# Optimization experiments

Measured on AMD Instinct MI355X. Metric: run time of the kernel, lower is better.

Reference implementation:

```python
import jax, jax.numpy as jnp
import numpy as np

N, H, B = 8192, 32, 4          # points, hypotheses, scenes
C0, C1, CF = 128, 128, 64      # scale-0 chans, scale-1 chans, pts_feat chans
HID = 256                      # h_dim
D0, D1 = 24, 48                # voxel grid sides per scale
EPS = 1e-5


def setup_inputs() -> dict:
    key = jax.random.key(0)
    ks = jax.random.split(key, 30)
    nrm = lambda k, s, sc=1.0: jax.random.normal(k, s, jnp.float32) * sc
    in_dim = C0 + C1 + CF
    inp = {
        'pts': jax.random.uniform(ks[0], (N, H, 3), jnp.float32),
        'pts_feat': nrm(ks[1], (N, H, CF)),
        'pts_batch': jax.random.randint(ks[2], (N,), 0, B),
        'vol0': nrm(ks[3], (B, C0, D0, D0, D0)),
        'vol1': nrm(ks[4], (B, C1, D1, D1, D1)),
        'w0': nrm(ks[5], (HID, in_dim, 3), 1.0 / np.sqrt(in_dim * 3)),
        'w1': nrm(ks[6], (HID, HID, 3), 1.0 / np.sqrt(HID * 3)),
        'w2': nrm(ks[7], (HID, HID, 3), 1.0 / np.sqrt(HID * 3)),
        'w3': nrm(ks[8], (1, HID, 3), 1.0 / np.sqrt(HID * 3)),
        'b3': jnp.zeros((1,), jnp.float32),
    }
    for i in range(3):
        k = jax.random.split(ks[9 + i], 4)
        inp[f'g{i}'] = 1.0 + 0.1 * nrm(k[0], (HID,))
        inp[f'b{i}'] = 0.1 * nrm(k[1], (HID,))
        inp[f'm{i}'] = 0.1 * nrm(k[2], (HID,))
        inp[f'v{i}'] = jax.random.uniform(k[3], (HID,), jnp.float32, 0.5, 1.5)
    return inp


def _trilinear(vol, coords, batch):
    """vol [B,C,X,Y,Z], coords [Q,3] in voxel units, batch [Q] -> [Q,C].
    Zero padding outside the grid; align_corners=True semantics."""
    Bv, C, X, Y, Z = vol.shape
    v = jnp.transpose(vol, (0, 2, 3, 4, 1))  # [B,X,Y,Z,C] channels-last gather
    dims = jnp.array([X, Y, Z], jnp.int32)
    f = jnp.floor(coords)
    frac = coords - f
    fi = f.astype(jnp.int32)
    out = jnp.zeros((coords.shape[0], C), vol.dtype)
    for dx in (0, 1):
        for dy in (0, 1):
            for dz in (0, 1):
                off = jnp.array([dx, dy, dz], jnp.int32)
                idx = fi + off
                valid = jnp.all((idx >= 0) & (idx < dims), axis=1)
                ic = jnp.clip(idx, 0, dims - 1)
                w = ((frac[:, 0] if dx else 1.0 - frac[:, 0]) *
                     (frac[:, 1] if dy else 1.0 - frac[:, 1]) *
                     (frac[:, 2] if dz else 1.0 - frac[:, 2]))
                g = v[batch, ic[:, 0], ic[:, 1], ic[:, 2]]  # [Q,C] irregular gather
                out = out + (w * valid.astype(w.dtype))[:, None] * g
    return out


def _conv1d(x, w):
    return jax.lax.conv_general_dilated(x, w, (1,), [(1, 1)],
                                        dimension_numbers=('NCH', 'OIH', 'NCH'))


def _bn(x, g, b, m, v):
    return (x - m[:, None]) * (g[:, None] / jnp.sqrt(v[:, None] + EPS)) + b[:, None]


def reference(pts, pts_feat, pts_batch, vol0, vol1,
              w0, g0, b0, m0, v0, w1, g1, b1, m1, v1,
              w2, g2, b2, m2, v2, w3, b3):
    n_pts, n_hyp = pts.shape[0], pts.shape[1]
    q = pts.reshape(-1, 3)                      # [N*H, 3], normalized [0,1]
    bidx = jnp.repeat(pts_batch, n_hyp)         # [N*H]
    f0 = _trilinear(vol0, q * (D0 - 1), bidx).reshape(n_pts, n_hyp, -1)
    f1 = _trilinear(vol1, q * (D1 - 1), bidx).reshape(n_pts, n_hyp, -1)
    # loop concatenation order: cat(f1, cat(f0, pts_feat))
    features = jnp.concatenate([f1, f0, pts_feat], axis=2)  # [N,H,320]
    x = jnp.transpose(features, (0, 2, 1))      # [N, 320, H]
    x = jax.nn.relu(_bn(_conv1d(x, w0), g0, b0, m0, v0))
    x = jax.nn.relu(_bn(_conv1d(x, w1), g1, b1, m1, v1))
    x = jax.nn.relu(_bn(_conv1d(x, w2), g2, b2, m2, v2))
    x = _conv1d(x, w3) + b3[None, :, None]      # [N,1,H]
    return jax.nn.softmax(x[:, 0, :], axis=1)   # [N,H]
```

## Files before the change

kernel.cpp:

```cpp
#include <hip/hip_runtime.h>


typedef _Float16 half8 __attribute__((ext_vector_type(8)));
typedef float floatx16 __attribute__((ext_vector_type(16)));

#define NPTS  8192
#define HH    32
#define GPTS  4
#define PITCH 324
#define S1    110592
#define S0    13824
#define EPSF  1e-5f

__global__ void tvol_h(const float* __restrict__ in, ushort* __restrict__ out, int S) {
    __shared__ float t[32][33];
    const int b  = blockIdx.z;
    const int s0 = blockIdx.x * 32, c0 = blockIdx.y * 32;
    const int tx = threadIdx.x & 31, ty = threadIdx.x >> 5;
    const float* ip = in + ((size_t)b * 128 + c0) * S + s0;
#pragma unroll
    for (int j = 0; j < 32; j += 8)
        t[ty + j][tx] = ip[(size_t)(ty + j) * S + tx];
    __syncthreads();
    ushort* op = out + ((size_t)b * S + s0) * 128 + c0;
#pragma unroll
    for (int j = 0; j < 32; j += 8)
        op[(size_t)(ty + j) * 128 + tx] = __builtin_bit_cast(ushort, (_Float16)t[tx][ty + j]);
}

__global__ void wprep(const float* __restrict__ w, ushort* __restrict__ dst, int I, int KC) {
    int tid = blockIdx.x * 256 + threadIdx.x;
    if (tid >= KC * 4096) return;
    int j    = tid & 7;
    int lane = (tid >> 3) & 63;
    int nt   = (tid >> 9) & 7;
    int kc   = tid >> 12;
    int I16  = I / 16;
    int o    = nt * 32 + (lane & 31);
    int t    = kc / I16;
    int iw   = (kc % I16) * 16 + (lane >> 5) * 8 + j;
    float v  = w[((size_t)o * I + iw) * 3 + t];
    dst[tid] = __builtin_bit_cast(ushort, (_Float16)v);
}

__device__ __forceinline__ void setup_corners(float px, float py, float pz, int D,
                                              int* __restrict__ idx, float* __restrict__ wt) {
    float cx = px * (D - 1), cy = py * (D - 1), cz = pz * (D - 1);
    float fx = floorf(cx), fy = floorf(cy), fz = floorf(cz);
    float rx = cx - fx, ry = cy - fy, rz = cz - fz;
    int ix = (int)fx, iy = (int)fy, iz = (int)fz;
#pragma unroll
    for (int k = 0; k < 8; ++k) {
        int dx = k >> 2, dy = (k >> 1) & 1, dz = k & 1;
        int jx = ix + dx, jy = iy + dy, jz = iz + dz;
        bool valid = (jx >= 0) && (jx < D) && (jy >= 0) && (jy < D) && (jz >= 0) && (jz < D);
        int cxi = min(max(jx, 0), D - 1), cyi = min(max(jy, 0), D - 1), czi = min(max(jz, 0), D - 1);
        float w = (dx ? rx : 1.f - rx) * (dy ? ry : 1.f - ry) * (dz ? rz : 1.f - rz);
        idx[k] = (cxi * D + cyi) * D + czi;
        wt[k]  = valid ? w : 0.f;
    }
}

__device__ __forceinline__ uint packh2(float a, float b) {
    ushort ua = __builtin_bit_cast(ushort, (_Float16)a);
    ushort ub = __builtin_bit_cast(ushort, (_Float16)b);
    return (uint)ua | ((uint)ub << 16);
}

__device__ __forceinline__ half8 lda(const ushort* p) {
    uint2 lo = *(const uint2*)p;
    uint2 hi = *(const uint2*)(p + 4);
    uint4 u; u.x = lo.x; u.y = lo.y; u.z = hi.x; u.w = hi.y;
    return __builtin_bit_cast(half8, u);
}

template <int I16>
__device__ __forceinline__ void conv_layer(
    ushort (&F)[GPTS][34][PITCH], const ushort* __restrict__ wf,
    const float* __restrict__ gg, const float* __restrict__ bb,
    const float* __restrict__ mm, const float* __restrict__ vv,
    int wv, int lane)
{
    constexpr int KC = 3 * I16;
    const int ch = wv * 32 + (lane & 31);
    const float sc = gg[ch] / sqrtf(vv[ch] + EPSF);
    const float bs = bb[ch] - mm[ch] * sc;

    floatx16 acc[GPTS];
#pragma unroll
    for (int p = 0; p < GPTS; ++p)
#pragma unroll
        for (int r = 0; r < 16; ++r) acc[p][r] = 0.f;

    const ushort* aB = &F[0][0][0] + (lane & 31) * PITCH + (lane >> 5) * 8;
    const ushort* bB = wf + (size_t)wv * 512 + (size_t)lane * 8;

    half8 p0 = *(const half8*)(bB);
    half8 p1 = *(const half8*)(bB + 1 * 4096);
    half8 p2 = *(const half8*)(bB + 2 * 4096);
    half8 p3 = *(const half8*)(bB + 3 * 4096);

    int t = 0, ic = 0;
#define STEP(BREG, KNEXT)                                                        \
    {                                                                            \
        const ushort* ap = aB + t * PITCH + ic * 16;                             \
        half8 a0 = lda(ap);                                                      \
        half8 a1 = lda(ap + 1 * 34 * PITCH);                                     \
        half8 a2 = lda(ap + 2 * 34 * PITCH);                                     \
        half8 a3 = lda(ap + 3 * 34 * PITCH);                                     \
        acc[0] = __builtin_amdgcn_mfma_f32_32x32x16_f16(a0, BREG, acc[0], 0, 0, 0); \
        acc[1] = __builtin_amdgcn_mfma_f32_32x32x16_f16(a1, BREG, acc[1], 0, 0, 0); \
        acc[2] = __builtin_amdgcn_mfma_f32_32x32x16_f16(a2, BREG, acc[2], 0, 0, 0); \
        acc[3] = __builtin_amdgcn_mfma_f32_32x32x16_f16(a3, BREG, acc[3], 0, 0, 0); \
        BREG = *(const half8*)(bB + (size_t)min(KNEXT, KC - 1) * 4096);          \
        if (++ic == I16) { ic = 0; ++t; }                                        \
    }

#pragma unroll 1
    for (int kc = 0; kc < KC; kc += 4) {
        STEP(p0, kc + 4)
        STEP(p1, kc + 5)
        STEP(p2, kc + 6)
        STEP(p3, kc + 7)
    }
#undef STEP

    __syncthreads();
#pragma unroll
    for (int p = 0; p < GPTS; ++p)
#pragma unroll
        for (int r = 0; r < 16; ++r) {
            int h = (r & 3) + 8 * (r >> 2) + 4 * (lane >> 5);
            float v = fmaxf(fmaf(acc[p][r], sc, bs), 0.f);
            F[p][h + 1][ch] = __builtin_bit_cast(ushort, (_Float16)v);
        }
    __syncthreads();
}

__global__ __launch_bounds__(512, 2) void fused_kernel(
    const float* __restrict__ pts, const float* __restrict__ pf,
    const int* __restrict__ pbatch,
    const ushort* __restrict__ v1t, const ushort* __restrict__ v0t,
    const ushort* __restrict__ wf0, const ushort* __restrict__ wf1,
    const ushort* __restrict__ wf2,
    const float* __restrict__ w3, const float* __restrict__ b3,
    const float* __restrict__ g0, const float* __restrict__ be0,
    const float* __restrict__ m0, const float* __restrict__ va0,
    const float* __restrict__ g1, const float* __restrict__ be1,
    const float* __restrict__ m1, const float* __restrict__ va1,
    const float* __restrict__ g2, const float* __restrict__ be2,
    const float* __restrict__ m2, const float* __restrict__ va2,
    float* __restrict__ outp)
{
    __shared__ ushort F[GPTS][34][PITCH];
    __shared__ float  w3s[768];

    const int tid = threadIdx.x, lane = tid & 63, wv = tid >> 6;

    if (tid < 256) {
        w3s[tid]       = w3[tid];
        w3s[256 + tid] = w3[256 + tid];
        w3s[512 + tid] = w3[512 + tid];
    }

    for (int i = tid; i < 162 * GPTS; i += 512) {
        int p = i / 162, c = i - p * 162;
        ((uint*)&F[p][0][0])[c]  = 0u;
        ((uint*)&F[p][33][0])[c] = 0u;
    }

    {
        const int g = tid >> 2, cj = tid & 3;
        const int pt = g >> 5, h = g & 31;
        const int n = blockIdx.x * GPTS + pt;
        const float* pp = pts + ((size_t)n * HH + h) * 3;
        const float px = pp[0], py = pp[1], pz = pp[2];
        const int bi = pbatch[n];
        int idx1[8]; float wt1[8]; setup_corners(px, py, pz, 48, idx1, wt1);
        int idx0[8]; float wt0[8]; setup_corners(px, py, pz, 24, idx0, wt0);

        {
            const ushort* vb = v1t + (size_t)bi * (128ull * S1) + cj * 32;
            float acc[32];
#pragma unroll
            for (int k = 0; k < 32; ++k) acc[k] = 0.f;
#pragma unroll
            for (int c = 0; c < 8; ++c) {
                const half8* p = (const half8*)(vb + (size_t)idx1[c] * 128);
                float w = wt1[c];
#pragma unroll
                for (int q = 0; q < 4; ++q) {
                    half8 x = p[q];
#pragma unroll
                    for (int e = 0; e < 8; ++e) acc[q * 8 + e] += w * (float)x[e];
                }
            }
            ushort* fr = &F[pt][h + 1][cj * 32];
#pragma unroll
            for (int k = 0; k < 8; ++k) {
                uint2 u; u.x = packh2(acc[4 * k], acc[4 * k + 1]);
                u.y = packh2(acc[4 * k + 2], acc[4 * k + 3]);
                ((uint2*)fr)[k] = u;
            }
        }
        {
            const ushort* vb = v0t + (size_t)bi * (128ull * S0) + cj * 32;
            float acc[32];
#pragma unroll
            for (int k = 0; k < 32; ++k) acc[k] = 0.f;
#pragma unroll
            for (int c = 0; c < 8; ++c) {
                const half8* p = (const half8*)(vb + (size_t)idx0[c] * 128);
                float w = wt0[c];
#pragma unroll
                for (int q = 0; q < 4; ++q) {
                    half8 x = p[q];
#pragma unroll
                    for (int e = 0; e < 8; ++e) acc[q * 8 + e] += w * (float)x[e];
                }
            }
            ushort* fr = &F[pt][h + 1][128 + cj * 32];
#pragma unroll
            for (int k = 0; k < 8; ++k) {
                uint2 u; u.x = packh2(acc[4 * k], acc[4 * k + 1]);
                u.y = packh2(acc[4 * k + 2], acc[4 * k + 3]);
                ((uint2*)fr)[k] = u;
            }
        }
        {
            const float* pfp = pf + ((size_t)n * HH + h) * 64 + cj * 16;
            ushort* fr = &F[pt][h + 1][256 + cj * 16];
#pragma unroll
            for (int k = 0; k < 4; ++k) {
                float4 v = *(const float4*)(pfp + 4 * k);
                uint2 u; u.x = packh2(v.x, v.y); u.y = packh2(v.z, v.w);
                ((uint2*)fr)[k] = u;
            }
        }
    }
    __syncthreads();

    conv_layer<20>(F, wf0, g0, be0, m0, va0, wv, lane);
    conv_layer<16>(F, wf1, g1, be1, m1, va1, wv, lane);
    conv_layer<16>(F, wf2, g2, be2, m2, va2, wv, lane);

    if (wv < GPTS) {
        const int hh = lane & 31, ihalf = lane >> 5;
        float a = 0.f;
#pragma unroll
        for (int t = 0; t < 3; ++t) {
            const ushort* fr = &F[wv][hh + t][ihalf * 128];
#pragma unroll
            for (int b8 = 0; b8 < 16; ++b8) {
                half8 x = lda(fr + b8 * 8);
                int i0 = ihalf * 128 + b8 * 8;
#pragma unroll
                for (int j = 0; j < 8; ++j)
                    a += (float)x[j] * w3s[(i0 + j) * 3 + t];
            }
        }
        a += __shfl_xor(a, 32, 64);
        a += b3[0];
        float mx = a;
#pragma unroll
        for (int m = 16; m >= 1; m >>= 1) mx = fmaxf(mx, __shfl_xor(mx, m, 64));
        float e = expf(a - mx);
        float s = e;
#pragma unroll
        for (int m = 16; m >= 1; m >>= 1) s += __shfl_xor(s, m, 64);
        if (lane < 32)
            outp[((size_t)(blockIdx.x * GPTS + wv)) * HH + hh] = e / s;
    }
}

extern "C" void kernel_launch(void* const* d_in, const int* in_sizes, int n_in,
                              void* d_out, int out_size, void* d_ws, size_t ws_size,
                              hipStream_t stream) {
    const float* pts      = (const float*)d_in[0];
    const float* pts_feat = (const float*)d_in[1];
    const int*   pbatch   = (const int*)d_in[2];
    const float* vol0     = (const float*)d_in[3];
    const float* vol1     = (const float*)d_in[4];
    const float* w0 = (const float*)d_in[5];
    const float* w1 = (const float*)d_in[6];
    const float* w2 = (const float*)d_in[7];
    const float* w3 = (const float*)d_in[8];
    const float* b3 = (const float*)d_in[9];
    const float* g0 = (const float*)d_in[10];
    const float* be0 = (const float*)d_in[11];
    const float* m0 = (const float*)d_in[12];
    const float* va0 = (const float*)d_in[13];
    const float* g1 = (const float*)d_in[14];
    const float* be1 = (const float*)d_in[15];
    const float* m1 = (const float*)d_in[16];
    const float* va1 = (const float*)d_in[17];
    const float* g2 = (const float*)d_in[18];
    const float* be2 = (const float*)d_in[19];
    const float* m2 = (const float*)d_in[20];
    const float* va2 = (const float*)d_in[21];
    float* outp = (float*)d_out;

    const size_t o_v1 = 0;
    const size_t s_v1 = 4ull * S1 * 128;
    const size_t o_v0 = o_v1 + s_v1;
    const size_t s_v0 = 4ull * S0 * 128;
    const size_t o_w0 = o_v0 + s_v0;
    const size_t s_w0 = 60ull * 4096;
    const size_t o_w1 = o_w0 + s_w0;
    const size_t s_w1 = 48ull * 4096;
    const size_t o_w2 = o_w1 + s_w1;
    const size_t s_w2 = 48ull * 4096;
    const size_t need = (o_w2 + s_w2) * 2 + 65536;
    if (ws_size < need) return;

    ushort* wsu = (ushort*)d_ws;
    ushort* v1t = wsu + o_v1;
    ushort* v0t = wsu + o_v0;
    ushort* wf0 = wsu + o_w0;
    ushort* wf1 = wsu + o_w1;
    ushort* wf2 = wsu + o_w2;

    tvol_h<<<dim3(S1 / 32, 4, 4), 256, 0, stream>>>(vol1, v1t, S1);
    tvol_h<<<dim3(S0 / 32, 4, 4), 256, 0, stream>>>(vol0, v0t, S0);
    wprep<<<(int)((60 * 4096 + 255) / 256), 256, 0, stream>>>(w0, wf0, 320, 60);
    wprep<<<(int)((48 * 4096 + 255) / 256), 256, 0, stream>>>(w1, wf1, 256, 48);
    wprep<<<(int)((48 * 4096 + 255) / 256), 256, 0, stream>>>(w2, wf2, 256, 48);

    fused_kernel<<<NPTS / GPTS, 512, 0, stream>>>(
        pts, pts_feat, pbatch, v1t, v0t, wf0, wf1, wf2, w3, b3,
        g0, be0, m0, va0, g1, be1, m1, va1, g2, be2, m2, va2, outp);
}
```

Measured before the change: 1.002 ms.

## Split gather from conv into separate kernels, shrink LDS tile for occupancy

Trilinear gathers and the pts_feat conversion move out of the fused kernel into a dedicated gather kernel that writes fp16 features to a workspace buffer, processed in chunks sized to the workspace. The conv kernel now handles 3 points per block with a padded pitch, 16-byte LDS loads and launch bounds allowing 4 blocks per CU, trading a global round-trip of the feature tensor for higher occupancy and no gather stalls inside the MFMA kernel. The volume transpose kernel is also rewritten to convert to fp16 before the LDS stage and emit 16-byte stores.

```diff
diff --git a/kernel.cpp b/kernel.cpp
--- a/kernel.cpp
+++ b/kernel.cpp
@@ -6,26 +6,42 @@
 
 #define NPTS  8192
 #define HH    32
-#define GPTS  4
-#define PITCH 324
+#define GPTS  3
+#define PITCH 328
+#define ROWS  34
 #define S1    110592
 #define S0    13824
 #define EPSF  1e-5f
 
-__global__ void tvol_h(const float* __restrict__ in, ushort* __restrict__ out, int S) {
-    __shared__ float t[32][33];
-    const int b  = blockIdx.z;
-    const int s0 = blockIdx.x * 32, c0 = blockIdx.y * 32;
-    const int tx = threadIdx.x & 31, ty = threadIdx.x >> 5;
-    const float* ip = in + ((size_t)b * 128 + c0) * S + s0;
-#pragma unroll
-    for (int j = 0; j < 32; j += 8)
-        t[ty + j][tx] = ip[(size_t)(ty + j) * S + tx];
+__global__ __launch_bounds__(256) void tvol2(const float* __restrict__ in,
+                                             ushort* __restrict__ out, int S) {
+    __shared__ uint t[64][65];
+    const int b  = blockIdx.y;
+    const int s0 = blockIdx.x * 64;
+    const int tid = threadIdx.x;
+    const int l = tid & 63, cp0 = tid >> 6;
+#pragma unroll
+    for (int rep = 0; rep < 16; ++rep) {
+        int cpi = cp0 + 4 * rep;
+        int c0 = 2 * cpi;
+        float x0 = in[((size_t)b * 128 + c0) * S + s0 + l];
+        float x1 = in[((size_t)b * 128 + c0 + 1) * S + s0 + l];
+        ushort u0 = __builtin_bit_cast(ushort, (_Float16)x0);
+        ushort u1 = __builtin_bit_cast(ushort, (_Float16)x1);
+        t[l][cpi] = (uint)u0 | ((uint)u1 << 16);
+    }
     __syncthreads();
-    ushort* op = out + ((size_t)b * S + s0) * 128 + c0;
-#pragma unroll
-    for (int j = 0; j < 32; j += 8)
-        op[(size_t)(ty + j) * 128 + tx] = __builtin_bit_cast(ushort, (_Float16)t[tx][ty + j]);
+    const int s = tid >> 2, qd = tid & 3;
+    uint4* op = (uint4*)(out + ((size_t)b * S + s0 + s) * 128 + qd * 32);
+#pragma unroll
+    for (int j = 0; j < 4; ++j) {
+        uint4 v;
+        v.x = t[s][qd * 16 + 4 * j + 0];
+        v.y = t[s][qd * 16 + 4 * j + 1];
+        v.z = t[s][qd * 16 + 4 * j + 2];
+        v.w = t[s][qd * 16 + 4 * j + 3];
+        op[j] = v;
+    }
 }
 
 __global__ void wprep(const float* __restrict__ w, ushort* __restrict__ dst, int I, int KC) {
@@ -67,16 +83,103 @@
     return (uint)ua | ((uint)ub << 16);
 }
 
-__device__ __forceinline__ half8 lda(const ushort* p) {
-    uint2 lo = *(const uint2*)p;
-    uint2 hi = *(const uint2*)(p + 4);
-    uint4 u; u.x = lo.x; u.y = lo.y; u.z = hi.x; u.w = hi.y;
+__device__ __forceinline__ half8 lda16(const ushort* p) {
+    uint4 u = *(const uint4*)p;
     return __builtin_bit_cast(half8, u);
+}
+
+__global__ __launch_bounds__(256, 4) void gather_kernel(
+    const float* __restrict__ pts, const float* __restrict__ pf,
+    const int* __restrict__ pbatch,
+    const ushort* __restrict__ v1t, const ushort* __restrict__ v0t,
+    ushort* __restrict__ Fg, int q0)
+{
+    const int gid  = blockIdx.x * 256 + threadIdx.x;
+    const int qrel = gid >> 2, cj = gid & 3;
+    const int q    = q0 + qrel;
+    const int n    = q >> 5;
+
+    const float* pp = pts + (size_t)q * 3;
+    const float px = pp[0], py = pp[1], pz = pp[2];
+    const int bi = pbatch[n];
+
+    int idx1[8]; float wt1[8]; setup_corners(px, py, pz, 48, idx1, wt1);
+    int idx0[8]; float wt0[8]; setup_corners(px, py, pz, 24, idx0, wt0);
+
+    ushort* dq = Fg + (size_t)qrel * 320;
+
+    {
+        const ushort* vb = v1t + (size_t)bi * (128ull * S1) + cj * 32;
+        float acc[32];
+#pragma unroll
+        for (int k = 0; k < 32; ++k) acc[k] = 0.f;
+#pragma unroll
+        for (int c = 0; c < 8; ++c) {
+            const ushort* p = vb + (size_t)idx1[c] * 128;
+            float w = wt1[c];
+#pragma unroll
+            for (int qd = 0; qd < 4; ++qd) {
+                half8 x = lda16(p + 8 * qd);
+#pragma unroll
+                for (int e = 0; e < 8; ++e) acc[qd * 8 + e] += w * (float)x[e];
+            }
+        }
+        uint4* d = (uint4*)(dq + cj * 32);
+#pragma unroll
+        for (int j = 0; j < 4; ++j) {
+            uint4 u;
+            u.x = packh2(acc[8 * j + 0], acc[8 * j + 1]);
+            u.y = packh2(acc[8 * j + 2], acc[8 * j + 3]);
+            u.z = packh2(acc[8 * j + 4], acc[8 * j + 5]);
+            u.w = packh2(acc[8 * j + 6], acc[8 * j + 7]);
+            d[j] = u;
+        }
+    }
+    {
+        const ushort* vb = v0t + (size_t)bi * (128ull * S0) + cj * 32;
+        float acc[32];
+#pragma unroll
+        for (int k = 0; k < 32; ++k) acc[k] = 0.f;
+#pragma unroll
+        for (int c = 0; c < 8; ++c) {
+            const ushort* p = vb + (size_t)idx0[c] * 128;
+            float w = wt0[c];
+#pragma unroll
+            for (int qd = 0; qd < 4; ++qd) {
+                half8 x = lda16(p + 8 * qd);
+#pragma unroll
+                for (int e = 0; e < 8; ++e) acc[qd * 8 + e] += w * (float)x[e];
+            }
+        }
+        uint4* d = (uint4*)(dq + 128 + cj * 32);
+#pragma unroll
+        for (int j = 0; j < 4; ++j) {
+            uint4 u;
+            u.x = packh2(acc[8 * j + 0], acc[8 * j + 1]);
+            u.y = packh2(acc[8 * j + 2], acc[8 * j + 3]);
+            u.z = packh2(acc[8 * j + 4], acc[8 * j + 5]);
+            u.w = packh2(acc[8 * j + 6], acc[8 * j + 7]);
+            d[j] = u;
+        }
+    }
+    {
+        const float* pfp = pf + (size_t)q * 64 + cj * 16;
+        uint4* d = (uint4*)(dq + 256 + cj * 16);
+#pragma unroll
+        for (int j = 0; j < 2; ++j) {
+            float4 a = ((const float4*)pfp)[2 * j];
+            float4 b = ((const float4*)pfp)[2 * j + 1];
+            uint4 u;
+            u.x = packh2(a.x, a.y); u.y = packh2(a.z, a.w);
+            u.z = packh2(b.x, b.y); u.w = packh2(b.z, b.w);
+            d[j] = u;
+        }
+    }
 }
 
 template <int I16>
 __device__ __forceinline__ void conv_layer(
-    ushort (&F)[GPTS][34][PITCH], const ushort* __restrict__ wf,
+    ushort (&F)[GPTS][ROWS][PITCH], const ushort* __restrict__ wf,
     const float* __restrict__ gg, const float* __restrict__ bb,
     const float* __restrict__ mm, const float* __restrict__ vv,
     int wv, int lane)
@@ -101,19 +204,17 @@
     half8 p3 = *(const half8*)(bB + 3 * 4096);
 
     int t = 0, ic = 0;
-#define STEP(BREG, KNEXT)                                                        \
-    {                                                                            \
-        const ushort* ap = aB + t * PITCH + ic * 16;                             \
-        half8 a0 = lda(ap);                                                      \
-        half8 a1 = lda(ap + 1 * 34 * PITCH);                                     \
-        half8 a2 = lda(ap + 2 * 34 * PITCH);                                     \
-        half8 a3 = lda(ap + 3 * 34 * PITCH);                                     \
+#define STEP(BREG, KNEXT)                                                           \
+    {                                                                               \
+        const ushort* ap = aB + t * PITCH + ic * 16;                                \
+        half8 a0 = lda16(ap);                                                       \
+        half8 a1 = lda16(ap + 1 * ROWS * PITCH);                                    \
+        half8 a2 = lda16(ap + 2 * ROWS * PITCH);                                    \
         acc[0] = __builtin_amdgcn_mfma_f32_32x32x16_f16(a0, BREG, acc[0], 0, 0, 0); \
         acc[1] = __builtin_amdgcn_mfma_f32_32x32x16_f16(a1, BREG, acc[1], 0, 0, 0); \
         acc[2] = __builtin_amdgcn_mfma_f32_32x32x16_f16(a2, BREG, acc[2], 0, 0, 0); \
-        acc[3] = __builtin_amdgcn_mfma_f32_32x32x16_f16(a3, BREG, acc[3], 0, 0, 0); \
-        BREG = *(const half8*)(bB + (size_t)min(KNEXT, KC - 1) * 4096);          \
-        if (++ic == I16) { ic = 0; ++t; }                                        \
+        BREG = *(const half8*)(bB + (size_t)min(KNEXT, KC - 1) * 4096);             \
+        if (++ic == I16) { ic = 0; ++t; }                                           \
     }
 
 #pragma unroll 1
@@ -137,10 +238,8 @@
     __syncthreads();
 }
 
-__global__ __launch_bounds__(512, 2) void fused_kernel(
-    const float* __restrict__ pts, const float* __restrict__ pf,
-    const int* __restrict__ pbatch,
-    const ushort* __restrict__ v1t, const ushort* __restrict__ v0t,
+__global__ __launch_bounds__(512, 4) void conv_kernel(
+    const ushort* __restrict__ Fg,
     const ushort* __restrict__ wf0, const ushort* __restrict__ wf1,
     const ushort* __restrict__ wf2,
     const float* __restrict__ w3, const float* __restrict__ b3,
@@ -150,93 +249,28 @@
     const float* __restrict__ m1, const float* __restrict__ va1,
     const float* __restrict__ g2, const float* __restrict__ be2,
     const float* __restrict__ m2, const float* __restrict__ va2,
-    float* __restrict__ outp)
+    float* __restrict__ outp, int startPt, int chunkPts)
 {
-    __shared__ ushort F[GPTS][34][PITCH];
-    __shared__ float  w3s[768];
+    __shared__ __align__(16) ushort F[GPTS][ROWS][PITCH];
+    __shared__ float w3s[768];
 
     const int tid = threadIdx.x, lane = tid & 63, wv = tid >> 6;
+    const int p0 = blockIdx.x * GPTS;
 
     if (tid < 256) {
         w3s[tid]       = w3[tid];
         w3s[256 + tid] = w3[256 + tid];
         w3s[512 + tid] = w3[512 + tid];
     }
-
-    for (int i = tid; i < 162 * GPTS; i += 512) {
-        int p = i / 162, c = i - p * 162;
-        ((uint*)&F[p][0][0])[c]  = 0u;
-        ((uint*)&F[p][33][0])[c] = 0u;
-    }
-
-    {
-        const int g = tid >> 2, cj = tid & 3;
-        const int pt = g >> 5, h = g & 31;
-        const int n = blockIdx.x * GPTS + pt;
-        const float* pp = pts + ((size_t)n * HH + h) * 3;
-        const float px = pp[0], py = pp[1], pz = pp[2];
-        const int bi = pbatch[n];
-        int idx1[8]; float wt1[8]; setup_corners(px, py, pz, 48, idx1, wt1);
-        int idx0[8]; float wt0[8]; setup_corners(px, py, pz, 24, idx0, wt0);
-
-        {
-            const ushort* vb = v1t + (size_t)bi * (128ull * S1) + cj * 32;
-            float acc[32];
-#pragma unroll
-            for (int k = 0; k < 32; ++k) acc[k] = 0.f;
-#pragma unroll
-            for (int c = 0; c < 8; ++c) {
-                const half8* p = (const half8*)(vb + (size_t)idx1[c] * 128);
-                float w = wt1[c];
-#pragma unroll
-                for (int q = 0; q < 4; ++q) {
-                    half8 x = p[q];
-#pragma unroll
-                    for (int e = 0; e < 8; ++e) acc[q * 8 + e] += w * (float)x[e];
-                }
-            }
-            ushort* fr = &F[pt][h + 1][cj * 32];
-#pragma unroll
-            for (int k = 0; k < 8; ++k) {
-                uint2 u; u.x = packh2(acc[4 * k], acc[4 * k + 1]);
-                u.y = packh2(acc[4 * k + 2], acc[4 * k + 3]);
-                ((uint2*)fr)[k] = u;
-            }
-        }
-        {
-            const ushort* vb = v0t + (size_t)bi * (128ull * S0) + cj * 32;
-            float acc[32];
-#pragma unroll
-            for (int k = 0; k < 32; ++k) acc[k] = 0.f;
-#pragma unroll
-            for (int c = 0; c < 8; ++c) {
-                const half8* p = (const half8*)(vb + (size_t)idx0[c] * 128);
-                float w = wt0[c];
-#pragma unroll
-                for (int q = 0; q < 4; ++q) {
-                    half8 x = p[q];
-#pragma unroll
-                    for (int e = 0; e < 8; ++e) acc[q * 8 + e] += w * (float)x[e];
-                }
-            }
-            ushort* fr = &F[pt][h + 1][128 + cj * 32];
-#pragma unroll
-            for (int k = 0; k < 8; ++k) {
-                uint2 u; u.x = packh2(acc[4 * k], acc[4 * k + 1]);
-                u.y = packh2(acc[4 * k + 2], acc[4 * k + 3]);
-                ((uint2*)fr)[k] = u;
-            }
-        }
-        {
-            const float* pfp = pf + ((size_t)n * HH + h) * 64 + cj * 16;
-            ushort* fr = &F[pt][h + 1][256 + cj * 16];
-#pragma unroll
-            for (int k = 0; k < 4; ++k) {
-                float4 v = *(const float4*)(pfp + 4 * k);
-                uint2 u; u.x = packh2(v.x, v.y); u.y = packh2(v.z, v.w);
-                ((uint2*)fr)[k] = u;
-            }
-        }
+    for (int i = tid; i < 984; i += 512) {
+        int pt = i / 328, rr = (i % 328) / 164, c = i % 164;
+        ((uint*)&F[pt][rr ? 33 : 0][0])[c] = 0u;
+    }
+    for (int i = tid; i < 3840; i += 512) {
+        int ql = i / 40, k = i % 40;
+        int ptl = min(p0 + (ql >> 5), chunkPts - 1);
+        const uint4* src = (const uint4*)(Fg + ((size_t)ptl * 32 + (ql & 31)) * 320 + k * 8);
+        *(uint4*)&F[ql >> 5][(ql & 31) + 1][k * 8] = *src;
     }
     __syncthreads();
 
@@ -252,7 +286,7 @@
             const ushort* fr = &F[wv][hh + t][ihalf * 128];
 #pragma unroll
             for (int b8 = 0; b8 < 16; ++b8) {
-                half8 x = lda(fr + b8 * 8);
+                half8 x = lda16(fr + b8 * 8);
                 int i0 = ihalf * 128 + b8 * 8;
 #pragma unroll
                 for (int j = 0; j < 8; ++j)
@@ -268,8 +302,10 @@
         float s = e;
 #pragma unroll
         for (int m = 16; m >= 1; m >>= 1) s += __shfl_xor(s, m, 64);
-        if (lane < 32)
-            outp[((size_t)(blockIdx.x * GPTS + wv)) * HH + hh] = e / s;
+        if (lane < 32) {
+            int n = startPt + min(p0 + wv, chunkPts - 1);
+            outp[(size_t)n * HH + hh] = e / s;
+        }
     }
 }
 
@@ -310,8 +346,14 @@
     const size_t s_w1 = 48ull * 4096;
     const size_t o_w2 = o_w1 + s_w1;
     const size_t s_w2 = 48ull * 4096;
-    const size_t need = (o_w2 + s_w2) * 2 + 65536;
-    if (ws_size < need) return;
+    const size_t o_fg = o_w2 + s_w2;
+
+    int chunks = 0;
+    for (int k = 1; k <= 32; k <<= 1) {
+        size_t fg = ((size_t)NPTS / k) * 32 * 320;
+        if ((o_fg + fg) * 2 <= ws_size) { chunks = k; break; }
+    }
+    if (!chunks) return;
 
     ushort* wsu = (ushort*)d_ws;
     ushort* v1t = wsu + o_v1;
@@ -319,14 +361,25 @@
     ushort* wf0 = wsu + o_w0;
     ushort* wf1 = wsu + o_w1;
     ushort* wf2 = wsu + o_w2;
-
-    tvol_h<<<dim3(S1 / 32, 4, 4), 256, 0, stream>>>(vol1, v1t, S1);
-    tvol_h<<<dim3(S0 / 32, 4, 4), 256, 0, stream>>>(vol0, v0t, S0);
+    ushort* Fg  = wsu + o_fg;
+
+    tvol2<<<dim3(S1 / 64, 4), 256, 0, stream>>>(vol1, v1t, S1);
+    tvol2<<<dim3(S0 / 64, 4), 256, 0, stream>>>(vol0, v0t, S0);
     wprep<<<(int)((60 * 4096 + 255) / 256), 256, 0, stream>>>(w0, wf0, 320, 60);
     wprep<<<(int)((48 * 4096 + 255) / 256), 256, 0, stream>>>(w1, wf1, 256, 48);
     wprep<<<(int)((48 * 4096 + 255) / 256), 256, 0, stream>>>(w2, wf2, 256, 48);
 
-    fused_kernel<<<NPTS / GPTS, 512, 0, stream>>>(
-        pts, pts_feat, pbatch, v1t, v0t, wf0, wf1, wf2, w3, b3,
-        g0, be0, m0, va0, g1, be1, m1, va1, g2, be2, m2, va2, outp);
-}
+    const int chunkPts = NPTS / chunks;
+    const int nq = chunkPts * HH;
+    const int gatherBlocks = nq / 64;
+    const int convBlocks = (chunkPts + GPTS - 1) / GPTS;
+    for (int c = 0; c < chunks; ++c) {
+        const int startPt = c * chunkPts;
+        gather_kernel<<<gatherBlocks, 256, 0, stream>>>(
+            pts, pts_feat, pbatch, v1t, v0t, Fg, startPt * HH);
+        conv_kernel<<<convBlocks, 512, 0, stream>>>(
+            Fg, wf0, wf1, wf2, w3, b3,
+            g0, be0, m0, va0, g1, be1, m1, va1, g2, be2, m2, va2,
+            outp, startPt, chunkPts);
+    }
+}
```

After: 1.344 ms. 1.34x slower.
